# Kernel tuning notes

Measured on AMD Instinct MI355X. Metric: run time of the kernel, lower is better.

The kernel has to match this reference:

```python
import jax, jax.numpy as jnp
import numpy as np

NUM_HEADS = 4
NUM_GROUPS = 8
EPS = 1e-5


def group_norm(x, w, b):
    # x: [N, C, H, W], normalize over (C//G, H, W) per group
    N, C, H, W = x.shape
    xg = x.reshape(N, NUM_GROUPS, C // NUM_GROUPS, H, W)
    mu = jnp.mean(xg, axis=(2, 3, 4), keepdims=True)
    var = jnp.var(xg, axis=(2, 3, 4), keepdims=True)
    xn = ((xg - mu) * jax.lax.rsqrt(var + EPS)).reshape(N, C, H, W)
    return xn * w[None, :, None, None] + b[None, :, None, None]


def conv1x1(x, w, b):
    # x: [N, C, H, W], w: [Cout, Cin], b: [Cout]
    return jnp.einsum('nchw,dc->ndhw', x, w) + b[None, :, None, None]


def setup_inputs() -> dict:
    key = jax.random.key(0)
    ks = jax.random.split(key, 12)
    N, C, H, W = 2, 256, 64, 64
    s = 1.0 / np.sqrt(C)
    inp = {
        'x': jax.random.normal(ks[0], (N, C, H, W), jnp.float32),
        'mask': jax.random.randint(ks[1], (N, 1, H, W), 0, 2, jnp.int32),
        'norm_w': jnp.ones((C,), jnp.float32),
        'norm_b': jnp.zeros((C,), jnp.float32),
        'q_w': jax.random.normal(ks[2], (C, C), jnp.float32) * s,
        'q_b': jnp.zeros((C,), jnp.float32),
        'k_w': jax.random.normal(ks[3], (C, C), jnp.float32) * s,
        'k_b': jnp.zeros((C,), jnp.float32),
        'v_w': jax.random.normal(ks[4], (C, C), jnp.float32) * s,
        'v_b': jnp.zeros((C,), jnp.float32),
        'p_w': jax.random.normal(ks[5], (C, C), jnp.float32) * s,
        'p_b': jnp.zeros((C,), jnp.float32),
    }
    return inp


def reference(x, mask, norm_w, norm_b, q_w, q_b, k_w, k_b, v_w, v_b, p_w, p_b):
    N, C, H, W = x.shape
    hd = C // NUM_HEADS  # head dim
    L = H * W
    xn = group_norm(x, norm_w, norm_b)
    q = conv1x1(xn, q_w, q_b).reshape(N, NUM_HEADS, hd, L)
    k = conv1x1(xn, k_w, k_b).reshape(N, NUM_HEADS, hd, L)
    v = conv1x1(xn, v_w, v_b).reshape(N, NUM_HEADS, hd, L)
    scores = jnp.einsum('nhcl,nhck->nhlk', q, k) * (hd ** -0.5)
    probs = jax.nn.softmax(scores, axis=-1)
    out = jnp.einsum('nhlk,nhck->nhcl', probs, v).reshape(N, C, H, W)
    out = conv1x1(out, p_w, p_b)
    return (x + out, mask)
```

## Files before the change

kernel.cpp:

```cpp
#include <hip/hip_runtime.h>
#include <hip/hip_bf16.h>

#define NBATCH 2
#define CCH    256
#define LLEN   4096
#define NGROUP 8
#define CPG    32
#define NHEAD  4
#define HD     64
#define GEPS   1e-5f
#define QSCALE 0.18033688011112042f


typedef short bf16x8 __attribute__((ext_vector_type(8)));
typedef float f32x4  __attribute__((ext_vector_type(4)));

__device__ __forceinline__ unsigned short f2b(float f) {
  unsigned u = __float_as_uint(f);
  u += 0x7FFFu + ((u >> 16) & 1u);
  return (unsigned short)(u >> 16);
}
__device__ __forceinline__ unsigned pack2bf(float a, float b) {
  __hip_bfloat162 h = __float22bfloat162_rn(make_float2(a, b));
  union { __hip_bfloat162 h; unsigned u; } c;
  c.h = h;
  return c.u;
}
__device__ __forceinline__ float exp2_(float x) {
#if __has_builtin(__builtin_amdgcn_exp2f)
  return __builtin_amdgcn_exp2f(x);
#else
  return exp2f(x);
#endif
}

__global__ __launch_bounds__(256) void setup_kernel(
    const float* __restrict__ qw, const float* __restrict__ kw,
    const float* __restrict__ vw, const float* __restrict__ pw,
    const float* __restrict__ qb, const float* __restrict__ kb,
    const float* __restrict__ vb, const float* __restrict__ pb,
    const float* __restrict__ x, const int* __restrict__ mask,
    unsigned short* __restrict__ w16, float* __restrict__ bias_ws,
    float* __restrict__ part, float* __restrict__ out2) {
  __shared__ float rs[4], rss[4];
  const int b = blockIdx.x;
  const int t = threadIdx.x;
  if (b < 256) {
    const int idx = b * 256 + t;
    const int m = idx >> 14;
    const int rem = idx & 16383;
    const int cout = rem >> 6;
    const int ch4 = (rem & 63) << 2;
    const float* src[4] = {qw, kw, vw, pw};
    const float sc = (m == 0) ? QSCALE : 1.0f;
    const float4 v = ((const float4*)src[m])[(size_t)cout * 64 + (ch4 >> 2)];
    unsigned short* dst = w16 +
        ((size_t)(m * 16 + (cout >> 4)) * 8 + (ch4 >> 5)) * 512 +
        ((cout & 15) + 16 * ((ch4 >> 3) & 3)) * 8 + (ch4 & 7);
    dst[0] = f2b(v.x * sc); dst[1] = f2b(v.y * sc);
    dst[2] = f2b(v.z * sc); dst[3] = f2b(v.w * sc);
    if (b == 0) {
      bias_ws[t]       = qb[t] * QSCALE;
      bias_ws[256 + t] = kb[t];
      bias_ws[512 + t] = vb[t];
      bias_ws[768 + t] = pb[t];
    }
  } else if (b < 512) {
    const int sb = b - 256;
    const int gidx = sb >> 4, sub = sb & 15;
    const float4* xp = (const float4*)(x + (size_t)gidx * (CPG * LLEN)) + (size_t)sub * 2048;
    float s = 0.f, ss = 0.f;
    for (int i = t; i < 2048; i += 256) {
      const float4 v = xp[i];
      s += v.x + v.y + v.z + v.w;
      ss = fmaf(v.x, v.x, ss);
      ss = fmaf(v.y, v.y, ss);
      ss = fmaf(v.z, v.z, ss);
      ss = fmaf(v.w, v.w, ss);
    }
#pragma unroll
    for (int off = 32; off; off >>= 1) {
      s  += __shfl_down(s, off);
      ss += __shfl_down(ss, off);
    }
    if ((t & 63) == 0) { rs[t >> 6] = s; rss[t >> 6] = ss; }
    __syncthreads();
    if (t == 0) {
      part[sb * 2 + 0] = rs[0] + rs[1] + rs[2] + rs[3];
      part[sb * 2 + 1] = rss[0] + rss[1] + rss[2] + rss[3];
    }
  } else {
    const int i = (b - 512) * 256 + t;
    out2[i] = (float)mask[i];
  }
}

__global__ __launch_bounds__(256) void gn_apply_kernel(const float* __restrict__ x,
                                                       const float* __restrict__ w,
                                                       const float* __restrict__ b,
                                                       const float* __restrict__ part,
                                                       unsigned short* __restrict__ xn16) {
  const int l0 = blockIdx.x * 64, c0 = blockIdx.y * 32, n = blockIdx.z;
  const int g16 = n * 8 + blockIdx.y;
  float s = 0.f, ss = 0.f;
#pragma unroll
  for (int i = 0; i < 16; i++) {
    s  += part[(g16 * 16 + i) * 2 + 0];
    ss += part[(g16 * 16 + i) * 2 + 1];
  }
  const float inv_cnt = 1.0f / (float)(CPG * LLEN);
  const float mu = s * inv_cnt;
  const float rsg = rsqrtf(ss * inv_cnt - mu * mu + GEPS);
  __shared__ float tile[32][68];
  const int t = threadIdx.x;
  const int cl = t >> 3, l8 = t & 7;
  const float aa = rsg * w[c0 + cl];
  const float dd = b[c0 + cl] - mu * aa;
  const float* xrow = x + ((size_t)n * CCH + c0 + cl) * LLEN + l0;
#pragma unroll
  for (int i = 0; i < 2; i++) {
    const int ll = (l8 + 8 * i) * 4;
    float4 v = *(const float4*)(xrow + ll);
    v.x = fmaf(v.x, aa, dd);
    v.y = fmaf(v.y, aa, dd);
    v.z = fmaf(v.z, aa, dd);
    v.w = fmaf(v.w, aa, dd);
    *(float4*)&tile[cl][ll] = v;
  }
  __syncthreads();
  const int l = t & 63, cg = t >> 6;
  const int labs = l0 + l;
  bf16x8 ov;
#pragma unroll
  for (int j = 0; j < 8; j++) ov[j] = (short)f2b(tile[cg * 8 + j][l]);
  const size_t pos = (((size_t)n * 256 + (labs >> 4)) * 8 + (c0 >> 5)) * 512 +
                     ((labs & 15) + 16 * cg) * 8;
  *(bf16x8*)(xn16 + pos) = ov;
}

__global__ __launch_bounds__(256, 4) void qkv_mfma_kernel(
    const unsigned short* __restrict__ xn16,
    const unsigned short* __restrict__ w16,
    const float* __restrict__ bias_ws,
    unsigned short* __restrict__ q16,
    unsigned short* __restrict__ k16,
    unsigned short* __restrict__ v16) {
  const int t = threadIdx.x;
  const int lane = t & 63, wv = t >> 6;
  const int col = lane & 15, quad = lane >> 4;
  const int m0 = blockIdx.x * 64;
  const int by = blockIdx.y;
  const int co0 = by * 64;
  const int wsel = blockIdx.z;
  const int n = m0 >> 12;
  const int m16b = (m0 & 4095) >> 4;

  const unsigned short* xnb = xn16 + (size_t)n * (256 * 8 * 512);
  const unsigned short* wb  = w16 + ((size_t)(wsel * 16 + by * 4 + wv) * 8) * 512 + lane * 8;

  f32x4 acc[4];
#pragma unroll
  for (int i = 0; i < 4; i++) acc[i] = {0.f, 0.f, 0.f, 0.f};

#pragma unroll
  for (int kc = 0; kc < 8; kc++) {
    const bf16x8 wf = *(const bf16x8*)(wb + (size_t)kc * 512);
#pragma unroll
    for (int mt = 0; mt < 4; mt++) {
      const bf16x8 xf = *(const bf16x8*)(xnb + ((size_t)(m16b + mt) * 8 + kc) * 512 + lane * 8);
      acc[mt] = (wsel < 2)
          ? __builtin_amdgcn_mfma_f32_16x16x32_bf16(xf, wf, acc[mt], 0, 0, 0)
          : __builtin_amdgcn_mfma_f32_16x16x32_bf16(wf, xf, acc[mt], 0, 0, 0);
    }
  }

  if (wsel < 2) {
    unsigned short* dst = (wsel == 0) ? q16 : k16;
    const float bias = bias_ws[wsel * CCH + co0 + wv * 16 + col];
    const int lquad = (wv * 2 + (col >> 3)) & 3;
    const int j = col & 7;
#pragma unroll
    for (int mt = 0; mt < 4; mt++) {
      const size_t base = ((size_t)(n * 256 + m16b + mt) * 8 + by * 2 + (wv >> 1)) * 512 + j;
#pragma unroll
      for (int r = 0; r < 4; r++)
        dst[base + ((quad * 4 + r) + 16 * lquad) * 8] = f2b(acc[mt][r] + bias);
    }
  } else {
    const int l0 = m0 & 4095;
    const int j = col & 7;
#pragma unroll
    for (int ct = 0; ct < 4; ct++) {
      const size_t base = ((size_t)(n * 128 + (l0 >> 5) + (ct >> 1)) * 16 + by * 4 + wv) * 512 +
                          16 * (((ct & 1) << 1) + (col >> 3)) * 8 + j;
#pragma unroll
      for (int r = 0; r < 4; r++) {
        const int cout = co0 + wv * 16 + quad * 4 + r;
        v16[base + (quad * 4 + r) * 8] = f2b(acc[ct][r] + bias_ws[2 * CCH + cout]);
      }
    }
  }
}

__global__ __launch_bounds__(256, 4) void attn_mfma_kernel(
    const unsigned short* __restrict__ q16,
    const unsigned short* __restrict__ k16,
    const unsigned short* __restrict__ v16,
    unsigned short* __restrict__ o16) {
  __shared__ __align__(16) unsigned char shraw[20480];
  unsigned short (*pT)[32][40] = (unsigned short (*)[32][40])shraw;
  f32x4 (*red)[4][64] = (f32x4 (*)[4][64])shraw;
  f32x4 (*lred)[64] = (f32x4 (*)[64])(shraw + 16384);
  const int t = threadIdx.x;
  const int lane = t & 63, wv = t >> 6;
  const int col = lane & 15, quad = lane >> 4;
  const int fid = blockIdx.y * gridDim.x + blockIdx.x;
  const int nh = fid & 7, qx = fid >> 3;
  const int n = nh >> 2, h = nh & 3;
  const int hc = h * HD;
  const int qt0 = qx * 2;

  const unsigned short* qb = q16 + (size_t)n * (256 * 8 * 512);
  const unsigned short* kb = k16 + (size_t)n * (256 * 8 * 512);
  const unsigned short* vb = v16 + (size_t)n * (128 * 16 * 512);

  bf16x8 bq[2][2];
#pragma unroll
  for (int qt = 0; qt < 2; qt++)
#pragma unroll
    for (int ks = 0; ks < 2; ks++)
      bq[qt][ks] = *(const bf16x8*)(qb + ((size_t)(qt0 + qt) * 8 + h * 2 + ks) * 512 + lane * 8);

  bf16x8 bones;
#pragma unroll
  for (int i = 0; i < 8; i++) bones[i] = (short)0x3F80;

  f32x4 o[2][4], lacc[2];
#pragma unroll
  for (int qt = 0; qt < 2; qt++) {
    lacc[qt] = {0.f, 0.f, 0.f, 0.f};
#pragma unroll
    for (int ct = 0; ct < 4; ct++) o[qt][ct] = {0.f, 0.f, 0.f, 0.f};
  }

  auto ldK = [&](int kc0, int kt, int ks) {
    return *(const bf16x8*)(kb + ((size_t)((kc0 >> 4) + kt) * 8 + h * 2 + ks) * 512 + lane * 8);
  };
  auto ldV = [&](int kc0, int ct) {
    return *(const bf16x8*)(vb + ((size_t)(kc0 >> 5) * 16 + h * 4 + ct) * 512 + lane * 8);
  };

  bf16x8 kA[2][2], kB[2][2], bv[4];
  auto loadK = [&](bf16x8 (&kr)[2][2], int kc0) {
#pragma unroll
    for (int kt = 0; kt < 2; kt++)
#pragma unroll
      for (int ks = 0; ks < 2; ks++) kr[kt][ks] = ldK(kc0, kt, ks);
  };
  auto loadV = [&](int kc0) {
#pragma unroll
    for (int ct = 0; ct < 4; ct++) bv[ct] = ldV(kc0, ct);
  };
  auto chunk = [&](bf16x8 (&kr)[2][2]) {
#pragma unroll
    for (int kt = 0; kt < 2; kt++)
#pragma unroll
      for (int qt = 0; qt < 2; qt++) {
        f32x4 s = {0.f, 0.f, 0.f, 0.f};
        s = __builtin_amdgcn_mfma_f32_16x16x32_bf16(kr[kt][0], bq[qt][0], s, 0, 0, 0);
        s = __builtin_amdgcn_mfma_f32_16x16x32_bf16(kr[kt][1], bq[qt][1], s, 0, 0, 0);
        uint2 pw;
        pw.x = pack2bf(exp2_(s[0]), exp2_(s[1]));
        pw.y = pack2bf(exp2_(s[2]), exp2_(s[3]));
        *(uint2*)&pT[wv][qt * 16 + col][kt * 16 + quad * 4] = pw;
      }
#pragma unroll
    for (int qt = 0; qt < 2; qt++) {
      const bf16x8 pa = *(const bf16x8*)&pT[wv][qt * 16 + col][quad * 8];
      lacc[qt] = __builtin_amdgcn_mfma_f32_16x16x32_bf16(pa, bones, lacc[qt], 0, 0, 0);
#pragma unroll
      for (int ct = 0; ct < 4; ct++)
        o[qt][ct] = __builtin_amdgcn_mfma_f32_16x16x32_bf16(pa, bv[ct], o[qt][ct], 0, 0, 0);
    }
  };

  const int kb0 = wv * 1024;
  loadK(kA, kb0);
  for (int it = 0; it < 32; it += 2) {
    loadV(kb0 + it * 32);
    loadK(kB, kb0 + (it + 1) * 32);
    chunk(kA);
    loadV(kb0 + (it + 1) * 32);
    loadK(kA, kb0 + ((it + 2 < 32) ? (it + 2) * 32 : (it + 1) * 32));
    chunk(kB);
  }

  const int cch = hc + wv * 16 + col;
  const int lquad16 = 16 * ((cch >> 3) & 3);
  const size_t ctile = cch >> 5;
#pragma unroll
  for (int qt = 0; qt < 2; qt++) {
    __syncthreads();
#pragma unroll
    for (int ct = 0; ct < 4; ct++) red[wv][ct][lane] = o[qt][ct];
    lred[wv][lane] = lacc[qt];
    __syncthreads();
    f32x4 os = red[0][wv][lane];
    os += red[1][wv][lane];
    os += red[2][wv][lane];
    os += red[3][wv][lane];
    f32x4 ls = lred[0][lane];
    ls += lred[1][lane];
    ls += lred[2][lane];
    ls += lred[3][lane];
    const size_t base = (((size_t)n * 256 + qt0 + qt) * 8 + ctile) * 512 + (cch & 7);
#pragma unroll
    for (int r = 0; r < 4; r++)
      o16[base + ((quad * 4 + r) + lquad16) * 8] = f2b(os[r] / ls[r]);
  }
}

__global__ __launch_bounds__(256, 4) void proj_mfma_kernel(
    const unsigned short* __restrict__ o16,
    const unsigned short* __restrict__ w16,
    const float* __restrict__ pbias,
    const float* __restrict__ x,
    float* __restrict__ out) {
  const int t = threadIdx.x;
  const int lane = t & 63, wv = t >> 6;
  const int col = lane & 15, quad = lane >> 4;
  const int m0 = blockIdx.x * 32;
  const int by = blockIdx.y;
  const int co0 = by * 64;
  const int n = m0 >> 12, l0 = m0 & 4095;

  const unsigned short* ob = o16 + (size_t)n * (256 * 8 * 512);
  const unsigned short* wb = w16 + ((size_t)(48 + by * 4 + wv) * 8) * 512 + lane * 8;

  f32x4 acc[2];
#pragma unroll
  for (int i = 0; i < 2; i++) acc[i] = {0.f, 0.f, 0.f, 0.f};

#pragma unroll
  for (int kc = 0; kc < 8; kc++) {
    const bf16x8 aw = *(const bf16x8*)(wb + (size_t)kc * 512);
#pragma unroll
    for (int lt = 0; lt < 2; lt++) {
      const bf16x8 bo = *(const bf16x8*)(ob + ((size_t)((l0 >> 4) + lt) * 8 + kc) * 512 + lane * 8);
      acc[lt] = __builtin_amdgcn_mfma_f32_16x16x32_bf16(aw, bo, acc[lt], 0, 0, 0);
    }
  }
#pragma unroll
  for (int lt = 0; lt < 2; lt++)
#pragma unroll
    for (int r = 0; r < 4; r++) {
      const int cout = co0 + wv * 16 + quad * 4 + r;
      const size_t idx = ((size_t)(n * CCH + cout)) * LLEN + l0 + lt * 16 + col;
      out[idx] = acc[lt][r] + pbias[cout] + x[idx];
    }
}

extern "C" void kernel_launch(void* const* d_in, const int* in_sizes, int n_in,
                              void* d_out, int out_size, void* d_ws, size_t ws_size,
                              hipStream_t stream) {
  (void)in_sizes; (void)n_in; (void)out_size; (void)ws_size;
  const float* x      = (const float*)d_in[0];
  const int*   mask   = (const int*)d_in[1];
  const float* norm_w = (const float*)d_in[2];
  const float* norm_b = (const float*)d_in[3];
  const float* q_w    = (const float*)d_in[4];
  const float* q_b    = (const float*)d_in[5];
  const float* k_w    = (const float*)d_in[6];
  const float* k_b    = (const float*)d_in[7];
  const float* v_w    = (const float*)d_in[8];
  const float* v_b    = (const float*)d_in[9];
  const float* p_w    = (const float*)d_in[10];
  const float* p_b    = (const float*)d_in[11];

  const size_t TSZ = (size_t)NBATCH * LLEN * CCH;
  unsigned short* xn16 = (unsigned short*)d_ws;
  unsigned short* q16  = xn16 + TSZ;
  unsigned short* k16  = q16 + TSZ;
  unsigned short* v16  = k16 + TSZ;
  unsigned short* o16  = v16 + TSZ;
  unsigned short* w16  = o16 + TSZ;
  float* bias_ws = (float*)(w16 + 4 * 65536);
  float* part    = bias_ws + 1024;

  float* out  = (float*)d_out;
  float* out2 = out + TSZ;

  setup_kernel<<<544, 256, 0, stream>>>(q_w, k_w, v_w, p_w, q_b, k_b, v_b, p_b,
                                        x, mask, w16, bias_ws, part, out2);
  gn_apply_kernel<<<dim3(LLEN / 64, CCH / 32, NBATCH), 256, 0, stream>>>(
      x, norm_w, norm_b, part, xn16);
  qkv_mfma_kernel<<<dim3((NBATCH * LLEN) / 64, CCH / 64, 3), 256, 0, stream>>>(
      xn16, w16, bias_ws, q16, k16, v16);
  attn_mfma_kernel<<<dim3(LLEN / 32, NBATCH * NHEAD), 256, 0, stream>>>(
      q16, k16, v16, o16);
  proj_mfma_kernel<<<dim3((NBATCH * LLEN) / 32, CCH / 64), 256, 0, stream>>>(
      o16, w16, bias_ws + 768, x, out);
}
```

Before: 156.0 us.

## Double query tile per attention block and transpose probabilities via permlane swaps

Each attention block now handles four 16-row query tiles instead of two, which halves the grid and reuses every K/V load for twice as many queries. The LDS round-trip that transposed exp'd scores into MFMA A-operand layout is replaced by in-register permlane32/permlane16 swaps. V loads are double-buffered alongside K, and s_setprio is raised around the PV MFMA burst. The cost is more registers per thread (launch bounds lowered to 2 waves per SIMD) and fewer blocks to spread across the GPU.

```diff
diff --git a/kernel.cpp b/kernel.cpp
--- a/kernel.cpp
+++ b/kernel.cpp
@@ -202,13 +202,12 @@
   }
 }
 
-__global__ __launch_bounds__(256, 4) void attn_mfma_kernel(
+__global__ __launch_bounds__(256, 2) void attn_mfma_kernel(
     const unsigned short* __restrict__ q16,
     const unsigned short* __restrict__ k16,
     const unsigned short* __restrict__ v16,
     unsigned short* __restrict__ o16) {
   __shared__ __align__(16) unsigned char shraw[20480];
-  unsigned short (*pT)[32][40] = (unsigned short (*)[32][40])shraw;
   f32x4 (*red)[4][64] = (f32x4 (*)[4][64])shraw;
   f32x4 (*lred)[64] = (f32x4 (*)[64])(shraw + 16384);
   const int t = threadIdx.x;
@@ -218,15 +217,15 @@
   const int nh = fid & 7, qx = fid >> 3;
   const int n = nh >> 2, h = nh & 3;
   const int hc = h * HD;
-  const int qt0 = qx * 2;
+  const int qt0 = qx * 4;
 
   const unsigned short* qb = q16 + (size_t)n * (256 * 8 * 512);
   const unsigned short* kb = k16 + (size_t)n * (256 * 8 * 512);
   const unsigned short* vb = v16 + (size_t)n * (128 * 16 * 512);
 
-  bf16x8 bq[2][2];
-#pragma unroll
-  for (int qt = 0; qt < 2; qt++)
+  bf16x8 bq[4][2];
+#pragma unroll
+  for (int qt = 0; qt < 4; qt++)
 #pragma unroll
     for (int ks = 0; ks < 2; ks++)
       bq[qt][ks] = *(const bf16x8*)(qb + ((size_t)(qt0 + qt) * 8 + h * 2 + ks) * 512 + lane * 8);
@@ -235,9 +234,9 @@
 #pragma unroll
   for (int i = 0; i < 8; i++) bones[i] = (short)0x3F80;
 
-  f32x4 o[2][4], lacc[2];
-#pragma unroll
-  for (int qt = 0; qt < 2; qt++) {
+  f32x4 o[4][4], lacc[4];
+#pragma unroll
+  for (int qt = 0; qt < 4; qt++) {
     lacc[qt] = {0.f, 0.f, 0.f, 0.f};
 #pragma unroll
     for (int ct = 0; ct < 4; ct++) o[qt][ct] = {0.f, 0.f, 0.f, 0.f};
@@ -250,56 +249,77 @@
     return *(const bf16x8*)(vb + ((size_t)(kc0 >> 5) * 16 + h * 4 + ct) * 512 + lane * 8);
   };
 
-  bf16x8 kA[2][2], kB[2][2], bv[4];
+  bf16x8 kA[2][2], kB[2][2], vA[4], vB[4];
   auto loadK = [&](bf16x8 (&kr)[2][2], int kc0) {
 #pragma unroll
     for (int kt = 0; kt < 2; kt++)
 #pragma unroll
       for (int ks = 0; ks < 2; ks++) kr[kt][ks] = ldK(kc0, kt, ks);
   };
-  auto loadV = [&](int kc0) {
-#pragma unroll
-    for (int ct = 0; ct < 4; ct++) bv[ct] = ldV(kc0, ct);
+  auto loadV = [&](bf16x8 (&vv)[4], int kc0) {
+#pragma unroll
+    for (int ct = 0; ct < 4; ct++) vv[ct] = ldV(kc0, ct);
   };
-  auto chunk = [&](bf16x8 (&kr)[2][2]) {
-#pragma unroll
-    for (int kt = 0; kt < 2; kt++)
-#pragma unroll
-      for (int qt = 0; qt < 2; qt++) {
+
+  auto chunk = [&](bf16x8 (&kr)[2][2], bf16x8 (&vv)[4]) {
+    bf16x8 pa[4];
+#pragma unroll
+    for (int qt = 0; qt < 4; qt++) {
+      unsigned a0, a1, b0, b1;
+      {
         f32x4 s = {0.f, 0.f, 0.f, 0.f};
-        s = __builtin_amdgcn_mfma_f32_16x16x32_bf16(kr[kt][0], bq[qt][0], s, 0, 0, 0);
-        s = __builtin_amdgcn_mfma_f32_16x16x32_bf16(kr[kt][1], bq[qt][1], s, 0, 0, 0);
-        uint2 pw;
-        pw.x = pack2bf(exp2_(s[0]), exp2_(s[1]));
-        pw.y = pack2bf(exp2_(s[2]), exp2_(s[3]));
-        *(uint2*)&pT[wv][qt * 16 + col][kt * 16 + quad * 4] = pw;
+        s = __builtin_amdgcn_mfma_f32_16x16x32_bf16(kr[0][0], bq[qt][0], s, 0, 0, 0);
+        s = __builtin_amdgcn_mfma_f32_16x16x32_bf16(kr[0][1], bq[qt][1], s, 0, 0, 0);
+        a0 = pack2bf(exp2_(s[0]), exp2_(s[1]));
+        a1 = pack2bf(exp2_(s[2]), exp2_(s[3]));
       }
-#pragma unroll
-    for (int qt = 0; qt < 2; qt++) {
-      const bf16x8 pa = *(const bf16x8*)&pT[wv][qt * 16 + col][quad * 8];
-      lacc[qt] = __builtin_amdgcn_mfma_f32_16x16x32_bf16(pa, bones, lacc[qt], 0, 0, 0);
+      {
+        f32x4 s = {0.f, 0.f, 0.f, 0.f};
+        s = __builtin_amdgcn_mfma_f32_16x16x32_bf16(kr[1][0], bq[qt][0], s, 0, 0, 0);
+        s = __builtin_amdgcn_mfma_f32_16x16x32_bf16(kr[1][1], bq[qt][1], s, 0, 0, 0);
+        b0 = pack2bf(exp2_(s[0]), exp2_(s[1]));
+        b1 = pack2bf(exp2_(s[2]), exp2_(s[3]));
+      }
+      auto r0 = __builtin_amdgcn_permlane32_swap(a0, b0, false, false);
+      auto s0 = __builtin_amdgcn_permlane16_swap(r0[0], r0[1], false, false);
+      auto r1 = __builtin_amdgcn_permlane32_swap(a1, b1, false, false);
+      auto s1 = __builtin_amdgcn_permlane16_swap(r1[0], r1[1], false, false);
+      union { unsigned u[4]; bf16x8 v; } pu;
+      pu.u[0] = s0[0];
+      pu.u[1] = s1[0];
+      pu.u[2] = s0[1];
+      pu.u[3] = s1[1];
+      pa[qt] = pu.v;
+    }
+    __builtin_amdgcn_s_setprio(1);
+#pragma unroll
+    for (int qt = 0; qt < 4; qt++) {
+      lacc[qt] = __builtin_amdgcn_mfma_f32_16x16x32_bf16(pa[qt], bones, lacc[qt], 0, 0, 0);
 #pragma unroll
       for (int ct = 0; ct < 4; ct++)
-        o[qt][ct] = __builtin_amdgcn_mfma_f32_16x16x32_bf16(pa, bv[ct], o[qt][ct], 0, 0, 0);
-    }
+        o[qt][ct] = __builtin_amdgcn_mfma_f32_16x16x32_bf16(pa[qt], vv[ct], o[qt][ct], 0, 0, 0);
+    }
+    __builtin_amdgcn_s_setprio(0);
   };
 
   const int kb0 = wv * 1024;
   loadK(kA, kb0);
+  loadV(vA, kb0);
   for (int it = 0; it < 32; it += 2) {
-    loadV(kb0 + it * 32);
     loadK(kB, kb0 + (it + 1) * 32);
-    chunk(kA);
-    loadV(kb0 + (it + 1) * 32);
-    loadK(kA, kb0 + ((it + 2 < 32) ? (it + 2) * 32 : (it + 1) * 32));
-    chunk(kB);
+    loadV(vB, kb0 + (it + 1) * 32);
+    chunk(kA, vA);
+    const int nx = (it + 2 < 32) ? (it + 2) : (it + 1);
+    loadK(kA, kb0 + nx * 32);
+    loadV(vA, kb0 + nx * 32);
+    chunk(kB, vB);
   }
 
   const int cch = hc + wv * 16 + col;
   const int lquad16 = 16 * ((cch >> 3) & 3);
   const size_t ctile = cch >> 5;
 #pragma unroll
-  for (int qt = 0; qt < 2; qt++) {
+  for (int qt = 0; qt < 4; qt++) {
     __syncthreads();
 #pragma unroll
     for (int ct = 0; ct < 4; ct++) red[wv][ct][lane] = o[qt][ct];
@@ -396,7 +416,7 @@
       x, norm_w, norm_b, part, xn16);
   qkv_mfma_kernel<<<dim3((NBATCH * LLEN) / 64, CCH / 64, 3), 256, 0, stream>>>(
       xn16, w16, bias_ws, q16, k16, v16);
-  attn_mfma_kernel<<<dim3(LLEN / 32, NBATCH * NHEAD), 256, 0, stream>>>(
+  attn_mfma_kernel<<<dim3(LLEN / 64, NBATCH * NHEAD), 256, 0, stream>>>(
       q16, k16, v16, o16);
   proj_mfma_kernel<<<dim3((NBATCH * LLEN) / 32, CCH / 64), 256, 0, stream>>>(
       o16, w16, bias_ws + 768, x, out);
```

After: 148.5 us. -4.8%, faster.
